# Performance work log

Hardware: AMD Instinct MI355X
Metric: run time of the kernel (lower is better)

Reference implementation:

```python
import jax, jax.numpy as jnp
import numpy as np

B, D_IN, H, HV, A, E, HW = 16384, 512, 512, 256, 32, 8, 512

def _lin(key, fan_in, fan_out):
    k1, k2 = jax.random.split(key)
    s = 1.0 / np.sqrt(fan_in)
    W = jax.random.uniform(k1, (fan_in, fan_out), minval=-s, maxval=s, dtype=jnp.float32)
    b = jax.random.uniform(k2, (fan_out,), minval=-s, maxval=s, dtype=jnp.float32)
    return W, b

def _stack(key, n, fan_in, fan_out):
    Ws, bs = [], []
    for k in jax.random.split(key, n):
        W, b = _lin(k, fan_in, fan_out)
        Ws.append(W); bs.append(b)
    return jnp.stack(Ws), jnp.stack(bs)

def setup_inputs() -> dict:
    key = jax.random.key(0)
    ks = jax.random.split(key, 16)
    x = jax.random.normal(ks[0], (B, D_IN), dtype=jnp.float32)
    # stacked expert policy nets: in->H, H->H, H->A (tanh)
    Wp0, bp0 = _stack(ks[1], E, D_IN, H)
    Wp1, bp1 = _stack(ks[2], E, H, H)
    Wmu, bmu = _stack(ks[3], E, H, A)
    # stacked expert value nets (hardcoded 256 hidden in source): in->256, 256->256, 256->1
    Wv0, bv0 = _stack(ks[4], E, D_IN, HV)
    Wv1, bv1 = _stack(ks[5], E, HV, HV)
    Wv, bv = _stack(ks[6], E, HV, 1)
    # gating net: in->HW, HW->HW, HW->E, softmax
    Ww0, bw0 = _lin(ks[7], D_IN, HW)
    Ww1, bw1 = _lin(ks[8], HW, HW)
    Wwo, bwo = _lin(ks[9], HW, E)
    return dict(x=x, Wp0=Wp0, bp0=bp0, Wp1=Wp1, bp1=bp1, Wmu=Wmu, bmu=bmu,
                Wv0=Wv0, bv0=bv0, Wv1=Wv1, bv1=bv1, Wv=Wv, bv=bv,
                Ww0=Ww0, bw0=bw0, Ww1=Ww1, bw1=bw1, Wwo=Wwo, bwo=bwo)

def reference(x, Wp0, bp0, Wp1, bp1, Wmu, bmu, Wv0, bv0, Wv1, bv1, Wv, bv,
              Ww0, bw0, Ww1, bw1, Wwo, bwo):
    # experts as one grouped/batched GEMM over axis e
    h = jax.nn.relu(jnp.einsum('bi,eih->ebh', x, Wp0) + bp0[:, None, :])      # [E,B,H]
    h = jax.nn.relu(jnp.einsum('ebh,ehk->ebk', h, Wp1) + bp1[:, None, :])
    actions = jnp.tanh(jnp.einsum('ebh,eha->eba', h, Wmu) + bmu[:, None, :])  # [E,B,A]
    # per-expert values
    g = jax.nn.relu(jnp.einsum('bi,eih->ebh', x, Wv0) + bv0[:, None, :])      # [E,B,HV]
    g = jax.nn.relu(jnp.einsum('ebh,ehk->ebk', g, Wv1) + bv1[:, None, :])
    values = jnp.einsum('ebh,eho->ebo', g, Wv) + bv[:, None, :]               # [E,B,1]
    # gating network + softmax
    u = jax.nn.relu(x @ Ww0 + bw0)
    u = jax.nn.relu(u @ Ww1 + bw1)
    w = jax.nn.softmax(u @ Wwo + bwo, axis=-1)                                # [B,E]
    # Categorical(w).sample() with a fixed key, then per-row gather of values
    pis = jax.random.categorical(jax.random.key(42), jnp.log(w), axis=-1)     # [B] int
    v = values[pis, jnp.arange(values.shape[1])]                              # [B,1]
    return actions, v, w
```

## Files before the change

### kernel.cpp

```cpp
#include <hip/hip_runtime.h>


typedef float   f32x4 __attribute__((ext_vector_type(4)));
typedef _Float16 f16;
typedef _Float16 f16x4 __attribute__((ext_vector_type(4)));
typedef _Float16 f16x8 __attribute__((ext_vector_type(8)));

typedef __attribute__((address_space(1))) unsigned int gas_u32;
typedef __attribute__((address_space(3))) unsigned int las_u32;

__device__ __forceinline__ void gl_lds16(const void* g, void* l) {
  __builtin_amdgcn_global_load_lds((gas_u32*)g, (las_u32*)l, 16, 0, 0);
}

__device__ __forceinline__ int xcd_swz(int b, int G) {
  int q = G >> 3, r = G & 7;
  int x = b & 7, y = b >> 3;
  return (x < r ? x * (q + 1) : r * (q + 1) + (x - r) * q) + y;
}

template<int BM, int BN, int WM, int WN, int EPI>
__global__ __launch_bounds__(256, 2) void gemm2_kernel(
    const f16* __restrict__ A, const f16* __restrict__ BT,
    const float* __restrict__ bias, void* __restrict__ Cv,
    const int K, const int lda, const int ldc,
    const long long sAe, const long long sCe,
    const int mT, const int nInner, const int eShift)
{
  constexpr int FM = WM / 16, FN = WN / 16;
  constexpr int WAVES_N = BN / WN;
  constexpr int HB = (BM + BN) * 128;
  __shared__ __align__(16) char sm[2 * HB];

  const int tid = threadIdx.x;
  const int lane = tid & 63;
  const int wid = tid >> 6;

  const int L = xcd_swz(blockIdx.x, gridDim.x);
  const int nIn = L % nInner;
  const int m = (L / nInner) % mT;
  const int eo = L / (nInner * mT);
  const int nv0 = (eo * nInner + nIn) * BN;
  const int e = nv0 >> eShift;
  const int col0 = nv0 & ((1 << eShift) - 1);
  const int m0 = m * BM;

  const f16* Ab = A + (size_t)sAe * e + (size_t)m0 * lda;
  const f16* Bb = BT + (size_t)nv0 * K;
  const int wr = wid / WAVES_N, wc = wid % WAVES_N;

  auto stage = [&](char* buf, int kt) {
    const f16* Ak = Ab + (kt << 6);
    const f16* Bk = Bb + (kt << 6);
    char* Ash = buf;
    char* Bsh = buf + BM * 128;
    #pragma unroll
    for (int u0 = 0; u0 < BM * 8; u0 += 256) {
      int u = u0 + tid;
      int row = u >> 3;
      int kb = ((u & 7) << 4) ^ ((row & 7) << 4);
      gl_lds16(Ak + (size_t)row * lda + (kb >> 1), Ash + u * 16);
    }
    #pragma unroll
    for (int u0 = 0; u0 < BN * 8; u0 += 256) {
      int u = u0 + tid;
      int row = u >> 3;
      int kb = ((u & 7) << 4) ^ ((row & 7) << 4);
      gl_lds16(Bk + (size_t)row * K + (kb >> 1), Bsh + u * 16);
    }
  };

  f32x4 acc[FM][FN] = {};
  const int ksteps = K >> 6;

  stage(sm, 0);
  __syncthreads();

  for (int kt = 0; kt < ksteps; ++kt) {
    char* cbuf = sm + (kt & 1) * HB;
    char* nbuf = sm + ((kt & 1) ^ 1) * HB;
    if (kt + 1 < ksteps) stage(nbuf, kt + 1);

    const char* Ash = cbuf;
    const char* Bsh = cbuf + BM * 128;
    f16x8 af[FM][2], bf[FN][2];
    const int kl = (lane >> 4) << 4;
    #pragma unroll
    for (int fm = 0; fm < FM; ++fm) {
      int row = wr * WM + fm * 16 + (lane & 15);
      int sw = (row & 7) << 4;
      af[fm][0] = *(const f16x8*)(Ash + row * 128 + (kl ^ sw));
      af[fm][1] = *(const f16x8*)(Ash + row * 128 + ((64 + kl) ^ sw));
    }
    #pragma unroll
    for (int fn = 0; fn < FN; ++fn) {
      int row = wc * WN + fn * 16 + (lane & 15);
      int sw = (row & 7) << 4;
      bf[fn][0] = *(const f16x8*)(Bsh + row * 128 + (kl ^ sw));
      bf[fn][1] = *(const f16x8*)(Bsh + row * 128 + ((64 + kl) ^ sw));
    }
    #pragma unroll
    for (int fm = 0; fm < FM; ++fm)
      #pragma unroll
      for (int fn = 0; fn < FN; ++fn) {
        acc[fm][fn] = __builtin_amdgcn_mfma_f32_16x16x32_f16(
            bf[fn][0], af[fm][0], acc[fm][fn], 0, 0, 0);
        acc[fm][fn] = __builtin_amdgcn_mfma_f32_16x16x32_f16(
            bf[fn][1], af[fm][1], acc[fm][fn], 0, 0, 0);
      }
    __syncthreads();
  }

  const int rbase = m0 + wr * WM + (lane & 15);
  const int cb = wc * WN + ((lane >> 4) << 2);
  #pragma unroll
  for (int fm = 0; fm < FM; ++fm) {
    const int row = rbase + fm * 16;
    #pragma unroll
    for (int fn = 0; fn < FN; ++fn) {
      const int bcol = cb + fn * 16;
      const int col = col0 + bcol;
      f32x4 v = acc[fm][fn];
      f32x4 bb = *(const f32x4*)(bias + nv0 + bcol);
      if constexpr (EPI == 0) {
        f16x4 h;
        #pragma unroll
        for (int r = 0; r < 4; ++r) h[r] = (f16)fmaxf(v[r] + bb[r], 0.0f);
        *(f16x4*)((f16*)Cv + (size_t)sCe * e + (size_t)row * ldc + col) = h;
      } else if constexpr (EPI == 1) {
        f32x4 o;
        #pragma unroll
        for (int r = 0; r < 4; ++r) o[r] = tanhf(v[r] + bb[r]);
        *(f32x4*)((float*)Cv + (size_t)sCe * e + (size_t)row * ldc + col) = o;
      } else if constexpr (EPI == 2) {
        f32x4 o;
        #pragma unroll
        for (int r = 0; r < 4; ++r) o[r] = fmaxf(v[r] + bb[r], 0.0f);
        *(f32x4*)((float*)Cv + (size_t)sCe * e + (size_t)row * ldc + col) = o;
      } else {
        f16x4 h, l, s;
        #pragma unroll
        for (int r = 0; r < 4; ++r) {
          float u = fmaxf(v[r] + bb[r], 0.0f);
          f16 hh = (f16)u;
          float hv = (float)hh;
          h[r] = hh;
          l[r] = (f16)((u - hv) * 32.0f);
          s[r] = (f16)(hv * 0.03125f);
        }
        f16* cp = (f16*)Cv + (size_t)row * ldc + col;
        *(f16x4*)(cp) = h;
        *(f16x4*)(cp + 512) = l;
        *(f16x4*)(cp + 1024) = s;
      }
    }
  }
}

__global__ __launch_bounds__(256) void prep_kernel(
    const float* __restrict__ x, f16* __restrict__ xsplit,
    const float* __restrict__ Wp0, f16* __restrict__ Wp0T,
    const float* __restrict__ Wp1, f16* __restrict__ Wp1T,
    const float* __restrict__ Wmu, f16* __restrict__ WmuT,
    const float* __restrict__ Wv0, f16* __restrict__ Wv0T,
    const float* __restrict__ Wv1, f16* __restrict__ Wv1T,
    const float* __restrict__ Ww0, f16* __restrict__ Ww0T3,
    const float* __restrict__ Ww1, f16* __restrict__ Ww1T3)
{
  __shared__ float t[32][33];
  const int tid = threadIdx.x;
  int b = blockIdx.x;
  if (b < 8192) {
    const size_t i = ((size_t)b * 256 + tid) * 4;
    const int row = (int)(i >> 9);
    const int col = (int)(i & 511);
    f32x4 v = *(const f32x4*)(x + i);
    f16x4 h, l, s;
    #pragma unroll
    for (int j = 0; j < 4; ++j) {
      f16 hh = (f16)v[j];
      float hv = (float)hh;
      h[j] = hh;
      l[j] = (f16)((v[j] - hv) * 32.0f);
      s[j] = (f16)(hv * 0.03125f);
    }
    f16* p = xsplit + (size_t)row * 1536 + col;
    *(f16x4*)(p) = h;
    *(f16x4*)(p + 512) = l;
    *(f16x4*)(p + 1024) = s;
    return;
  }
  b -= 8192;
  const float* W;
  f16* T;
  bool triple = false;
  int K, N;
  if (b < 2048)               { W = Wp0; T = Wp0T; K = 512; N = 512; }
  else if ((b -= 2048) < 2048){ W = Wp1; T = Wp1T; K = 512; N = 512; }
  else if ((b -= 2048) < 128) { W = Wmu; T = WmuT; K = 512; N = 32; }
  else if ((b -= 128) < 1024) { W = Wv0; T = Wv0T; K = 512; N = 256; }
  else if ((b -= 1024) < 512) { W = Wv1; T = Wv1T; K = 256; N = 256; }
  else if ((b -= 512) < 256)  { W = Ww0; T = Ww0T3; triple = true; K = 512; N = 512; }
  else { b -= 256;              W = Ww1; T = Ww1T3; triple = true; K = 512; N = 512; }

  const int kT = K >> 5, nT = N >> 5;
  const int e = b / (kT * nT);
  const int rem = b % (kT * nT);
  const int k0 = (rem % kT) << 5;
  const int n0 = (rem / kT) << 5;
  const int tx = tid & 31, ty = tid >> 5;
  const float* Wp = W + (size_t)e * K * N;
  #pragma unroll
  for (int i = 0; i < 4; ++i)
    t[ty + i * 8][tx] = Wp[(size_t)(k0 + ty + i * 8) * N + n0 + tx];
  __syncthreads();
  #pragma unroll
  for (int i = 0; i < 4; ++i) {
    const int n = n0 + ty + i * 8, k = k0 + tx;
    float v = t[tx][ty + i * 8];
    f16 hh = (f16)v;
    if (!triple) {
      T[(size_t)e * K * N + (size_t)n * K + k] = hh;
    } else {
      float hv = (float)hh;
      f16* p = T + (size_t)n * 1536 + k;
      p[0] = hh;
      p[512] = (f16)(hv * 0.03125f);
      p[1024] = (f16)((v - hv) * 32.0f);
    }
  }
}

__global__ __launch_bounds__(256) void values_kernel(
    const f16* __restrict__ G2, const float* __restrict__ Wv,
    const float* __restrict__ bv, float* __restrict__ values, const int e0)
{
  const int tid = threadIdx.x, lane = tid & 63, wid = tid >> 6;
  const int gi = blockIdx.x * 4 + wid;
  const int el = gi >> 14;
  const int b = gi & 16383;
  const int eg = e0 + el;
  const f16* g = G2 + (((size_t)el << 14) + b) * 256 + (lane << 2);
  f16x4 gv = *(const f16x4*)g;
  const float* wv = Wv + ((size_t)eg << 8) + (lane << 2);
  float a = (float)gv[0] * wv[0] + (float)gv[1] * wv[1] +
            (float)gv[2] * wv[2] + (float)gv[3] * wv[3];
  #pragma unroll
  for (int off = 32; off >= 1; off >>= 1) a += __shfl_xor(a, off);
  if (lane == 0) values[((size_t)eg << 14) + b] = a + bv[eg];
}

__device__ __forceinline__ void threefry_0_42(unsigned x0, unsigned x1,
                                              unsigned& o0, unsigned& o1)
{
  const unsigned ks0 = 0u, ks1 = 42u, ks2 = 0x1BD11BDAu ^ 42u;
  x0 += ks0; x1 += ks1;
#define TF_R(r) { x0 += x1; x1 = (x1 << r) | (x1 >> (32 - r)); x1 ^= x0; }
  TF_R(13) TF_R(15) TF_R(26) TF_R(6)  x0 += ks1; x1 += ks2 + 1u;
  TF_R(17) TF_R(29) TF_R(16) TF_R(24) x0 += ks2; x1 += ks0 + 2u;
  TF_R(13) TF_R(15) TF_R(26) TF_R(6)  x0 += ks0; x1 += ks1 + 3u;
  TF_R(17) TF_R(29) TF_R(16) TF_R(24) x0 += ks1; x1 += ks2 + 4u;
  TF_R(13) TF_R(15) TF_R(26) TF_R(6)  x0 += ks2; x1 += ks0 + 5u;
#undef TF_R
  o0 = x0; o1 = x1;
}

__global__ __launch_bounds__(256) void gating_out_kernel(
    const float* __restrict__ U2, const float* __restrict__ Wwo,
    const float* __restrict__ bwo, const float* __restrict__ values,
    float* __restrict__ w_out, float* __restrict__ v_out)
{
  __shared__ float wl[4096];
  const int tid = threadIdx.x;
  for (int i = tid; i < 1024; i += 256)
    ((f32x4*)wl)[i] = ((const f32x4*)Wwo)[i];
  __syncthreads();
  const int lane = tid & 63, wid = tid >> 6;
  const int b = blockIdx.x * 4 + wid;

  const float* u = U2 + (size_t)b * 512 + lane * 8;
  f32x4 ua = *(const f32x4*)u;
  f32x4 ub = *(const f32x4*)(u + 4);
  float acc[8] = {};
  const float* wrow = wl + lane * 64;
  #pragma unroll
  for (int i = 0; i < 8; ++i) {
    float uv = (i < 4) ? ua[i] : ub[i - 4];
    #pragma unroll
    for (int ee = 0; ee < 8; ++ee) acc[ee] += uv * wrow[i * 8 + ee];
  }
  #pragma unroll
  for (int off = 32; off >= 1; off >>= 1)
    #pragma unroll
    for (int ee = 0; ee < 8; ++ee) acc[ee] += __shfl_xor(acc[ee], off);
  #pragma unroll
  for (int ee = 0; ee < 8; ++ee) acc[ee] += bwo[ee];

  float zmax = acc[0];
  #pragma unroll
  for (int ee = 1; ee < 8; ++ee) zmax = fmaxf(zmax, acc[ee]);
  float s = 0.0f;
  #pragma unroll
  for (int ee = 0; ee < 8; ++ee) s += expf(acc[ee] - zmax);

  float t0 = (lane & 1) ? acc[1] : acc[0];
  float t1 = (lane & 1) ? acc[3] : acc[2];
  float t2 = (lane & 1) ? acc[5] : acc[4];
  float t3 = (lane & 1) ? acc[7] : acc[6];
  float s0 = (lane & 2) ? t1 : t0;
  float s1 = (lane & 2) ? t3 : t2;
  float zown = (lane & 4) ? s1 : s0;

  if (lane < 8) w_out[(size_t)b * 8 + lane] = expf(zown - zmax) / s;

  unsigned idx = ((unsigned)b << 3) | (unsigned)(lane & 7);
  unsigned o0, o1;
  threefry_0_42(0u, idx, o0, o1);
  unsigned bits = o0 ^ o1;
  float f = __uint_as_float((bits >> 9) | 0x3F800000u) - 1.0f;
  f = fmaxf(f, 1.17549435e-38f);
  float g = -logf(-logf(f));
  float y = (lane < 8) ? (zown + g) : -3.0e38f;

  float best = __shfl(y, 0);
  int pi = 0;
  #pragma unroll
  for (int ee = 1; ee < 8; ++ee) {
    float ye = __shfl(y, ee);
    if (ye > best) { best = ye; pi = ee; }
  }
  if (lane == 0) v_out[b] = values[((size_t)pi << 14) + b];
}

extern "C" void kernel_launch(void* const* d_in, const int* in_sizes, int n_in,
                              void* d_out, int out_size, void* d_ws, size_t ws_size,
                              hipStream_t stream) {
  (void)in_sizes; (void)n_in; (void)out_size;
  const float* x   = (const float*)d_in[0];
  const float* Wp0 = (const float*)d_in[1];
  const float* bp0 = (const float*)d_in[2];
  const float* Wp1 = (const float*)d_in[3];
  const float* bp1 = (const float*)d_in[4];
  const float* Wmu = (const float*)d_in[5];
  const float* bmu = (const float*)d_in[6];
  const float* Wv0 = (const float*)d_in[7];
  const float* bv0 = (const float*)d_in[8];
  const float* Wv1 = (const float*)d_in[9];
  const float* bv1 = (const float*)d_in[10];
  const float* Wv  = (const float*)d_in[11];
  const float* bv  = (const float*)d_in[12];
  const float* Ww0 = (const float*)d_in[13];
  const float* bw0 = (const float*)d_in[14];
  const float* Ww1 = (const float*)d_in[15];
  const float* bw1 = (const float*)d_in[16];
  const float* Wwo = (const float*)d_in[17];
  const float* bwo = (const float*)d_in[18];

  float* out_actions = (float*)d_out;
  float* out_v = out_actions + (size_t)8 * 16384 * 32;
  float* out_w = out_v + 16384;

  char* base = (char*)d_ws;
  size_t off = 0;
  auto alloc = [&](size_t bytes) -> char* {
    char* p = base + off;
    off = (off + bytes + 255) & ~(size_t)255;
    return p;
  };

  const size_t BD2 = (size_t)16384 * 512 * 2;
  const size_t BH2 = (size_t)16384 * 256 * 2;

  f16* xsplit = (f16*)alloc((size_t)16384 * 1536 * 2);
  f16* Wp0T   = (f16*)alloc((size_t)8 * 512 * 512 * 2);
  f16* Wp1T   = (f16*)alloc((size_t)8 * 512 * 512 * 2);
  f16* WmuT   = (f16*)alloc((size_t)8 * 32 * 512 * 2);
  f16* Wv0T   = (f16*)alloc((size_t)8 * 256 * 512 * 2);
  f16* Wv1T   = (f16*)alloc((size_t)8 * 256 * 256 * 2);
  f16* Ww0T3  = (f16*)alloc((size_t)512 * 1536 * 2);
  f16* Ww1T3  = (f16*)alloc((size_t)512 * 1536 * 2);
  float* valuesBuf = (float*)alloc((size_t)8 * 16384 * 4);

  size_t core = off;
  int eg = 8;
  while (eg > 1 && core + (size_t)2 * eg * BD2 > ws_size) eg >>= 1;
  const int eg_v = (2 * eg > 8) ? 8 : 2 * eg;

  f16 *BIG1, *BIG2, *U1split;
  float* U2;
  if (eg >= 4) {
    BIG1 = (f16*)alloc((size_t)eg * BD2);
    BIG2 = (f16*)alloc((size_t)eg * BD2);
    U1split = BIG1;
    U2 = (float*)BIG2;
  } else {
    BIG1 = (f16*)alloc((size_t)eg * BD2);
    BIG2 = (f16*)alloc((size_t)eg * BD2);
    U1split = (f16*)alloc((size_t)16384 * 1536 * 2);
    U2 = (float*)alloc((size_t)16384 * 512 * 4);
  }
  f16* VB1 = BIG1;
  f16* VB2 = (f16*)((char*)BIG1 + (size_t)eg_v * BH2);

  dim3 blk(256);
  const long long sBD = 16384LL * 512;
  const long long sBH = 16384LL * 256;

  prep_kernel<<<14464, blk, 0, stream>>>(
      x, xsplit, Wp0, Wp0T, Wp1, Wp1T, Wmu, WmuT, Wv0, Wv0T, Wv1, Wv1T,
      Ww0, Ww0T3, Ww1, Ww1T3);

  for (int e0 = 0; e0 < 8; e0 += eg) {
    gemm2_kernel<128, 128, 64, 64, 0><<<128 * 4 * eg, blk, 0, stream>>>(
        xsplit, Wp0T + (size_t)e0 * 512 * 512, bp0 + e0 * 512, BIG1,
        512, 1536, 512, 0, sBD, 128, 4 * eg, 9);
    gemm2_kernel<128, 128, 64, 64, 0><<<128 * 4 * eg, blk, 0, stream>>>(
        BIG1, Wp1T + (size_t)e0 * 512 * 512, bp1 + e0 * 512, BIG2,
        512, 512, 512, sBD, sBD, 128, 4, 9);
    gemm2_kernel<128, 32, 32, 32, 1><<<128 * eg, blk, 0, stream>>>(
        BIG2, WmuT + (size_t)e0 * 32 * 512, bmu + e0 * 32,
        out_actions + (size_t)e0 * 16384 * 32,
        512, 512, 32, sBD, 16384LL * 32, 128, 1, 5);
  }

  for (int e0 = 0; e0 < 8; e0 += eg_v) {
    gemm2_kernel<128, 128, 64, 64, 0><<<128 * 2 * eg_v, blk, 0, stream>>>(
        xsplit, Wv0T + (size_t)e0 * 256 * 512, bv0 + e0 * 256, VB1,
        512, 1536, 256, 0, sBH, 128, 2 * eg_v, 8);
    gemm2_kernel<128, 128, 64, 64, 0><<<128 * 2 * eg_v, blk, 0, stream>>>(
        VB1, Wv1T + (size_t)e0 * 256 * 256, bv1 + e0 * 256, VB2,
        256, 256, 256, sBH, sBH, 128, 2, 8);
    values_kernel<<<eg_v * 4096, blk, 0, stream>>>((const f16*)VB2, Wv, bv, valuesBuf, e0);
  }

  gemm2_kernel<128, 128, 64, 64, 3><<<512, blk, 0, stream>>>(
      xsplit, Ww0T3, bw0, U1split,
      1536, 1536, 1536, 0, 0, 128, 4, 9);
  gemm2_kernel<128, 128, 64, 64, 2><<<512, blk, 0, stream>>>(
      U1split, Ww1T3, bw1, U2,
      1536, 1536, 512, 0, 0, 128, 4, 9);
  gating_out_kernel<<<4096, blk, 0, stream>>>(U2, Wwo, bwo, valuesBuf, out_w, out_v);
}
```

Before: 484.2 us.

## Use 256x128 single-buffered GEMM tiles with 8 waves and restructure workspace batching

Adds a gemm3 kernel that uses 512-thread blocks with a 256x128 tile and a single LDS buffer, in place of the double-buffered 128x128 kernel. The aim is better operand reuse per block and more occupancy from the smaller LDS footprint. The policy first layer is now launched for all experts at once when the workspace is large enough, and the value nets run in a single pass over a fixed arena layout. Dropping double buffering exposes load latency, so overlap now depends on multiple resident blocks per CU, and the fixed workspace offsets assume a minimum workspace size.

```diff
diff --git a/kernel.cpp b/kernel.cpp
--- a/kernel.cpp
+++ b/kernel.cpp
@@ -19,22 +19,23 @@
   return (x < r ? x * (q + 1) : r * (q + 1) + (x - r) * q) + y;
 }
 
-template<int BM, int BN, int WM, int WN, int EPI>
-__global__ __launch_bounds__(256, 2) void gemm2_kernel(
+template<int EPI>
+__global__ __launch_bounds__(512, 4) void gemm3_kernel(
     const f16* __restrict__ A, const f16* __restrict__ BT,
     const float* __restrict__ bias, void* __restrict__ Cv,
     const int K, const int lda, const int ldc,
     const long long sAe, const long long sCe,
     const int mT, const int nInner, const int eShift)
 {
-  constexpr int FM = WM / 16, FN = WN / 16;
-  constexpr int WAVES_N = BN / WN;
-  constexpr int HB = (BM + BN) * 128;
-  __shared__ __align__(16) char sm[2 * HB];
+  constexpr int BM = 256, BN = 128;
+  __shared__ __align__(16) char sm[(BM + BN) * 128];
+  char* Ash = sm;
+  char* Bsh = sm + BM * 128;
 
   const int tid = threadIdx.x;
   const int lane = tid & 63;
   const int wid = tid >> 6;
+  const int wr = wid >> 1, wc = wid & 1;
 
   const int L = xcd_swz(blockIdx.x, gridDim.x);
   const int nIn = L % nInner;
@@ -47,77 +48,64 @@
 
   const f16* Ab = A + (size_t)sAe * e + (size_t)m0 * lda;
   const f16* Bb = BT + (size_t)nv0 * K;
-  const int wr = wid / WAVES_N, wc = wid % WAVES_N;
-
-  auto stage = [&](char* buf, int kt) {
+
+  f32x4 acc[4][4] = {};
+  const int ksteps = K >> 6;
+
+  for (int kt = 0; kt < ksteps; ++kt) {
+    __syncthreads();
     const f16* Ak = Ab + (kt << 6);
     const f16* Bk = Bb + (kt << 6);
-    char* Ash = buf;
-    char* Bsh = buf + BM * 128;
-    #pragma unroll
-    for (int u0 = 0; u0 < BM * 8; u0 += 256) {
+    #pragma unroll
+    for (int u0 = 0; u0 < BM * 8; u0 += 512) {
       int u = u0 + tid;
       int row = u >> 3;
       int kb = ((u & 7) << 4) ^ ((row & 7) << 4);
       gl_lds16(Ak + (size_t)row * lda + (kb >> 1), Ash + u * 16);
     }
     #pragma unroll
-    for (int u0 = 0; u0 < BN * 8; u0 += 256) {
+    for (int u0 = 0; u0 < BN * 8; u0 += 512) {
       int u = u0 + tid;
       int row = u >> 3;
       int kb = ((u & 7) << 4) ^ ((row & 7) << 4);
       gl_lds16(Bk + (size_t)row * K + (kb >> 1), Bsh + u * 16);
     }
-  };
-
-  f32x4 acc[FM][FN] = {};
-  const int ksteps = K >> 6;
-
-  stage(sm, 0);
-  __syncthreads();
-
-  for (int kt = 0; kt < ksteps; ++kt) {
-    char* cbuf = sm + (kt & 1) * HB;
-    char* nbuf = sm + ((kt & 1) ^ 1) * HB;
-    if (kt + 1 < ksteps) stage(nbuf, kt + 1);
-
-    const char* Ash = cbuf;
-    const char* Bsh = cbuf + BM * 128;
-    f16x8 af[FM][2], bf[FN][2];
+    __syncthreads();
+
+    f16x8 af[4][2], bf[4][2];
     const int kl = (lane >> 4) << 4;
     #pragma unroll
-    for (int fm = 0; fm < FM; ++fm) {
-      int row = wr * WM + fm * 16 + (lane & 15);
+    for (int fm = 0; fm < 4; ++fm) {
+      int row = wr * 64 + fm * 16 + (lane & 15);
       int sw = (row & 7) << 4;
       af[fm][0] = *(const f16x8*)(Ash + row * 128 + (kl ^ sw));
       af[fm][1] = *(const f16x8*)(Ash + row * 128 + ((64 + kl) ^ sw));
     }
     #pragma unroll
-    for (int fn = 0; fn < FN; ++fn) {
-      int row = wc * WN + fn * 16 + (lane & 15);
+    for (int fn = 0; fn < 4; ++fn) {
+      int row = wc * 64 + fn * 16 + (lane & 15);
       int sw = (row & 7) << 4;
       bf[fn][0] = *(const f16x8*)(Bsh + row * 128 + (kl ^ sw));
       bf[fn][1] = *(const f16x8*)(Bsh + row * 128 + ((64 + kl) ^ sw));
     }
     #pragma unroll
-    for (int fm = 0; fm < FM; ++fm)
+    for (int fm = 0; fm < 4; ++fm)
       #pragma unroll
-      for (int fn = 0; fn < FN; ++fn) {
+      for (int fn = 0; fn < 4; ++fn) {
         acc[fm][fn] = __builtin_amdgcn_mfma_f32_16x16x32_f16(
             bf[fn][0], af[fm][0], acc[fm][fn], 0, 0, 0);
         acc[fm][fn] = __builtin_amdgcn_mfma_f32_16x16x32_f16(
             bf[fn][1], af[fm][1], acc[fm][fn], 0, 0, 0);
       }
-    __syncthreads();
-  }
-
-  const int rbase = m0 + wr * WM + (lane & 15);
-  const int cb = wc * WN + ((lane >> 4) << 2);
-  #pragma unroll
-  for (int fm = 0; fm < FM; ++fm) {
+  }
+
+  const int rbase = m0 + wr * 64 + (lane & 15);
+  const int cb = wc * 64 + ((lane >> 4) << 2);
+  #pragma unroll
+  for (int fm = 0; fm < 4; ++fm) {
     const int row = rbase + fm * 16;
     #pragma unroll
-    for (int fn = 0; fn < FN; ++fn) {
+    for (int fn = 0; fn < 4; ++fn) {
       const int bcol = cb + fn * 16;
       const int col = col0 + bcol;
       f32x4 v = acc[fm][fn];
@@ -127,11 +115,6 @@
         #pragma unroll
         for (int r = 0; r < 4; ++r) h[r] = (f16)fmaxf(v[r] + bb[r], 0.0f);
         *(f16x4*)((f16*)Cv + (size_t)sCe * e + (size_t)row * ldc + col) = h;
-      } else if constexpr (EPI == 1) {
-        f32x4 o;
-        #pragma unroll
-        for (int r = 0; r < 4; ++r) o[r] = tanhf(v[r] + bb[r]);
-        *(f32x4*)((float*)Cv + (size_t)sCe * e + (size_t)row * ldc + col) = o;
       } else if constexpr (EPI == 2) {
         f32x4 o;
         #pragma unroll
@@ -148,10 +131,115 @@
           l[r] = (f16)((u - hv) * 32.0f);
           s[r] = (f16)(hv * 0.03125f);
         }
-        f16* cp = (f16*)Cv + (size_t)row * ldc + col;
+        f16* cp = (f16*)Cv + (size_t)sCe * e + (size_t)row * ldc + col;
         *(f16x4*)(cp) = h;
         *(f16x4*)(cp + 512) = l;
         *(f16x4*)(cp + 1024) = s;
+      }
+    }
+  }
+}
+
+template<int BM, int BN, int WM, int WN, int EPI>
+__global__ __launch_bounds__(256, 2) void gemm2_kernel(
+    const f16* __restrict__ A, const f16* __restrict__ BT,
+    const float* __restrict__ bias, void* __restrict__ Cv,
+    const int K, const int lda, const int ldc,
+    const long long sAe, const long long sCe,
+    const int mT, const int nInner, const int eShift)
+{
+  constexpr int FM = WM / 16, FN = WN / 16;
+  constexpr int WAVES_N = BN / WN;
+  __shared__ __align__(16) char sm[(BM + BN) * 128];
+  char* Ash = sm;
+  char* Bsh = sm + BM * 128;
+
+  const int tid = threadIdx.x;
+  const int lane = tid & 63;
+  const int wid = tid >> 6;
+
+  const int L = xcd_swz(blockIdx.x, gridDim.x);
+  const int nIn = L % nInner;
+  const int m = (L / nInner) % mT;
+  const int eo = L / (nInner * mT);
+  const int nv0 = (eo * nInner + nIn) * BN;
+  const int e = nv0 >> eShift;
+  const int col0 = nv0 & ((1 << eShift) - 1);
+  const int m0 = m * BM;
+
+  const f16* Ab = A + (size_t)sAe * e + (size_t)m0 * lda;
+  const f16* Bb = BT + (size_t)nv0 * K;
+  const int wr = wid / WAVES_N, wc = wid % WAVES_N;
+
+  f32x4 acc[FM][FN] = {};
+  const int ksteps = K >> 6;
+
+  for (int kt = 0; kt < ksteps; ++kt) {
+    __syncthreads();
+    const f16* Ak = Ab + (kt << 6);
+    const f16* Bk = Bb + (kt << 6);
+    for (int u0 = 0; u0 < BM * 8; u0 += 256) {
+      int u = u0 + tid;
+      int row = u >> 3;
+      int kb = ((u & 7) << 4) ^ ((row & 7) << 4);
+      gl_lds16(Ak + (size_t)row * lda + (kb >> 1), Ash + u * 16);
+    }
+    for (int u0 = 0; u0 < BN * 8; u0 += 256) {
+      int u = u0 + tid;
+      int row = u >> 3;
+      int kb = ((u & 7) << 4) ^ ((row & 7) << 4);
+      gl_lds16(Bk + (size_t)row * K + (kb >> 1), Bsh + u * 16);
+    }
+    __syncthreads();
+
+    f16x8 af[FM][2], bf[FN][2];
+    const int kl = (lane >> 4) << 4;
+    #pragma unroll
+    for (int fm = 0; fm < FM; ++fm) {
+      int row = wr * WM + fm * 16 + (lane & 15);
+      int sw = (row & 7) << 4;
+      af[fm][0] = *(const f16x8*)(Ash + row * 128 + (kl ^ sw));
+      af[fm][1] = *(const f16x8*)(Ash + row * 128 + ((64 + kl) ^ sw));
+    }
+    #pragma unroll
+    for (int fn = 0; fn < FN; ++fn) {
+      int row = wc * WN + fn * 16 + (lane & 15);
+      int sw = (row & 7) << 4;
+      bf[fn][0] = *(const f16x8*)(Bsh + row * 128 + (kl ^ sw));
+      bf[fn][1] = *(const f16x8*)(Bsh + row * 128 + ((64 + kl) ^ sw));
+    }
+    #pragma unroll
+    for (int fm = 0; fm < FM; ++fm)
+      #pragma unroll
+      for (int fn = 0; fn < FN; ++fn) {
+        acc[fm][fn] = __builtin_amdgcn_mfma_f32_16x16x32_f16(
+            bf[fn][0], af[fm][0], acc[fm][fn], 0, 0, 0);
+        acc[fm][fn] = __builtin_amdgcn_mfma_f32_16x16x32_f16(
+            bf[fn][1], af[fm][1], acc[fm][fn], 0, 0, 0);
+      }
+  }
+
+  const int rbase = m0 + wr * WM + (lane & 15);
+  const int cb = wc * WN + ((lane >> 4) << 2);
+  #pragma unroll
+  for (int fm = 0; fm < FM; ++fm) {
+    const int row = rbase + fm * 16;
+    #pragma unroll
+    for (int fn = 0; fn < FN; ++fn) {
+      const int bcol = cb + fn * 16;
+      const int col = col0 + bcol;
+      f32x4 v = acc[fm][fn];
+      f32x4 bb = *(const f32x4*)(bias + nv0 + bcol);
+      if constexpr (EPI == 0) {
+        f16x4 h;
+        #pragma unroll
+        for (int r = 0; r < 4; ++r) h[r] = (f16)fmaxf(v[r] + bb[r], 0.0f);
+        *(f16x4*)((f16*)Cv + (size_t)sCe * e + (size_t)row * ldc + col) = h;
+      } else {
+        f32x4 o;
+        #pragma unroll
+        for (int r = 0; r < 4; ++r) o[r] = tanhf(v[r] + bb[r]);
+        *(f32x4*)((float*)Cv + (size_t)sCe * e + (size_t)row * ldc + col) = o;
       }
     }
   }
@@ -368,9 +456,6 @@
     return p;
   };
 
-  const size_t BD2 = (size_t)16384 * 512 * 2;
-  const size_t BH2 = (size_t)16384 * 256 * 2;
-
   f16* xsplit = (f16*)alloc((size_t)16384 * 1536 * 2);
   f16* Wp0T   = (f16*)alloc((size_t)8 * 512 * 512 * 2);
   f16* Wp1T   = (f16*)alloc((size_t)8 * 512 * 512 * 2);
@@ -381,28 +466,21 @@
   f16* Ww1T3  = (f16*)alloc((size_t)512 * 1536 * 2);
   float* valuesBuf = (float*)alloc((size_t)8 * 16384 * 4);
 
-  size_t core = off;
-  int eg = 8;
-  while (eg > 1 && core + (size_t)2 * eg * BD2 > ws_size) eg >>= 1;
-  const int eg_v = (2 * eg > 8) ? 8 : 2 * eg;
-
-  f16 *BIG1, *BIG2, *U1split;
-  float* U2;
-  if (eg >= 4) {
-    BIG1 = (f16*)alloc((size_t)eg * BD2);
-    BIG2 = (f16*)alloc((size_t)eg * BD2);
-    U1split = BIG1;
-    U2 = (float*)BIG2;
-  } else {
-    BIG1 = (f16*)alloc((size_t)eg * BD2);
-    BIG2 = (f16*)alloc((size_t)eg * BD2);
-    U1split = (f16*)alloc((size_t)16384 * 1536 * 2);
-    U2 = (float*)alloc((size_t)16384 * 512 * 4);
-  }
-  f16* VB1 = BIG1;
-  f16* VB2 = (f16*)((char*)BIG1 + (size_t)eg_v * BH2);
+  char* arena = base + off;
+  const size_t avail = (ws_size > off) ? ws_size - off : 0;
+  const size_t SZ67  = (size_t)67108864;
+  const size_t SZ134 = (size_t)134217728;
+  const bool full = avail >= SZ134 + SZ67;
+
+  f16* P1 = (f16*)arena;
+  f16* P2 = (f16*)(arena + (full ? SZ134 : SZ67));
+  f16* VB1 = (f16*)arena;
+  f16* VB2 = (f16*)(arena + SZ67);
+  f16* U1split = (f16*)arena;
+  float* U2 = (float*)(arena + (size_t)50331648);
 
   dim3 blk(256);
+  dim3 blk8(512);
   const long long sBD = 16384LL * 512;
   const long long sBH = 16384LL * 256;
 
@@ -410,34 +488,42 @@
       x, xsplit, Wp0, Wp0T, Wp1, Wp1T, Wmu, WmuT, Wv0, Wv0T, Wv1, Wv1T,
       Ww0, Ww0T3, Ww1, Ww1T3);
 
-  for (int e0 = 0; e0 < 8; e0 += eg) {
-    gemm2_kernel<128, 128, 64, 64, 0><<<128 * 4 * eg, blk, 0, stream>>>(
-        xsplit, Wp0T + (size_t)e0 * 512 * 512, bp0 + e0 * 512, BIG1,
-        512, 1536, 512, 0, sBD, 128, 4 * eg, 9);
-    gemm2_kernel<128, 128, 64, 64, 0><<<128 * 4 * eg, blk, 0, stream>>>(
-        BIG1, Wp1T + (size_t)e0 * 512 * 512, bp1 + e0 * 512, BIG2,
-        512, 512, 512, sBD, sBD, 128, 4, 9);
-    gemm2_kernel<128, 32, 32, 32, 1><<<128 * eg, blk, 0, stream>>>(
-        BIG2, WmuT + (size_t)e0 * 32 * 512, bmu + e0 * 32,
-        out_actions + (size_t)e0 * 16384 * 32,
-        512, 512, 32, sBD, 16384LL * 32, 128, 1, 5);
-  }
-
-  for (int e0 = 0; e0 < 8; e0 += eg_v) {
-    gemm2_kernel<128, 128, 64, 64, 0><<<128 * 2 * eg_v, blk, 0, stream>>>(
-        xsplit, Wv0T + (size_t)e0 * 256 * 512, bv0 + e0 * 256, VB1,
-        512, 1536, 256, 0, sBH, 128, 2 * eg_v, 8);
-    gemm2_kernel<128, 128, 64, 64, 0><<<128 * 2 * eg_v, blk, 0, stream>>>(
-        VB1, Wv1T + (size_t)e0 * 256 * 256, bv1 + e0 * 256, VB2,
-        256, 256, 256, sBH, sBH, 128, 2, 8);
-    values_kernel<<<eg_v * 4096, blk, 0, stream>>>((const f16*)VB2, Wv, bv, valuesBuf, e0);
-  }
-
-  gemm2_kernel<128, 128, 64, 64, 3><<<512, blk, 0, stream>>>(
-      xsplit, Ww0T3, bw0, U1split,
-      1536, 1536, 1536, 0, 0, 128, 4, 9);
-  gemm2_kernel<128, 128, 64, 64, 2><<<512, blk, 0, stream>>>(
-      U1split, Ww1T3, bw1, U2,
-      1536, 1536, 512, 0, 0, 128, 4, 9);
+  if (full) {
+    gemm3_kernel<0><<<2048, blk8, 0, stream>>>(
+        xsplit, Wp0T, bp0, P1, 512, 1536, 512, 0, sBD, 64, 32, 9);
+    for (int e0 = 0; e0 < 8; e0 += 4) {
+      gemm3_kernel<0><<<1024, blk8, 0, stream>>>(
+          P1 + (size_t)e0 * sBD, Wp1T + (size_t)e0 * 512 * 512, bp1 + e0 * 512,
+          P2, 512, 512, 512, sBD, sBD, 64, 4, 9);
+      gemm2_kernel<128, 32, 32, 32, 1><<<512, blk, 0, stream>>>(
+          P2, WmuT + (size_t)e0 * 32 * 512, bmu + e0 * 32,
+          out_actions + (size_t)e0 * 16384 * 32,
+          512, 512, 32, sBD, 16384LL * 32, 128, 1, 5);
+    }
+  } else {
+    for (int e0 = 0; e0 < 8; e0 += 4) {
+      gemm3_kernel<0><<<1024, blk8, 0, stream>>>(
+          xsplit, Wp0T + (size_t)e0 * 512 * 512, bp0 + e0 * 512, P1,
+          512, 1536, 512, 0, sBD, 64, 16, 9);
+      gemm3_kernel<0><<<1024, blk8, 0, stream>>>(
+          P1, Wp1T + (size_t)e0 * 512 * 512, bp1 + e0 * 512, P2,
+          512, 512, 512, sBD, sBD, 64, 4, 9);
+      gemm2_kernel<128, 32, 32, 32, 1><<<512, blk, 0, stream>>>(
+          P2, WmuT + (size_t)e0 * 32 * 512, bmu + e0 * 32,
+          out_actions + (size_t)e0 * 16384 * 32,
+          512, 512, 32, sBD, 16384LL * 32, 128, 1, 5);
+    }
+  }
+
+  gemm3_kernel<0><<<1024, blk8, 0, stream>>>(
+      xsplit, Wv0T, bv0, VB1, 512, 1536, 256, 0, sBH, 64, 16, 8);
+  gemm3_kernel<0><<<1024, blk8, 0, stream>>>(
+      VB1, Wv1T, bv1, VB2, 256, 256, 256, sBH, sBH, 64, 2, 8);
+  values_kernel<<<32768, blk, 0, stream>>>((const f16*)VB2, Wv, bv, valuesBuf, 0);
+
+  gemm3_kernel<3><<<256, blk8, 0, stream>>>(
+      xsplit, Ww0T3, bw0, U1split, 1536, 1536, 1536, 0, 0, 64, 4, 9);
+  gemm3_kernel<2><<<256, blk8, 0, stream>>>(
+      U1split, Ww1T3, bw1, U2, 1536, 1536, 512, 0, 0, 64, 4, 9);
   gating_out_kernel<<<4096, blk, 0, stream>>>(U2, Wwo, bwo, valuesBuf, out_w, out_v);
 }
```

Result: slower. 499.8 us (+3.2%).
